# Optimization experiments

Measured on AMD Instinct MI355X. Metric: run time of the kernel, lower is better.

Reference implementation:

```python
import jax, jax.numpy as jnp
import numpy as np

B, S, D = 2, 2048, 1024
H = 16
HD = D // H  # 64
SCALE = HD ** -0.5
EPS = 1e-12  # F.normalize eps


def _rope_sin_cos(length, half, dtype):
    positions = jnp.arange(length, dtype=dtype)
    freqs = jnp.arange(half, dtype=dtype)
    inv_freq = 1.0 / 10000 ** (freqs / max(1, half))
    theta = jnp.einsum('s,f->sf', positions, inv_freq)  # [S, half]
    return jnp.sin(theta)[None, None], jnp.cos(theta)[None, None]  # [1,1,S,half]


def _rotate(x, sin, cos):
    # x: [B,H,S,HD]; interleaved even/odd rotation
    x_even = x[..., 0::2]
    x_odd = x[..., 1::2]
    r_even = x_even * cos - x_odd * sin
    r_odd = x_even * sin + x_odd * cos
    return jnp.stack([r_even, r_odd], axis=-1).reshape(x.shape)


def setup_inputs() -> dict:
    key = jax.random.key(0)
    k1, k2, k3 = jax.random.split(key, 3)
    tokens = jax.random.normal(k1, (B, S, D), dtype=jnp.float32)
    qkv_w = jax.random.normal(k2, (3 * D, D), dtype=jnp.float32) * (D ** -0.5)
    qkv_b = jnp.zeros((3 * D,), dtype=jnp.float32)
    out_w = jax.random.normal(k3, (D, D), dtype=jnp.float32) * (D ** -0.5)
    out_b = jnp.zeros((D,), dtype=jnp.float32)
    return {"tokens": tokens, "qkv_w": qkv_w, "qkv_b": qkv_b,
            "out_w": out_w, "out_b": out_b}


def reference(tokens, qkv_w, qkv_b, out_w, out_b):
    batch, length, _ = tokens.shape
    qkv = tokens @ qkv_w.T + qkv_b                       # [B,S,3D]
    qkv = qkv.reshape(batch, length, 3, H, HD)
    qkv = jnp.transpose(qkv, (0, 3, 1, 2, 4))            # [B,H,S,3,HD]
    q, k, v = qkv[..., 0, :], qkv[..., 1, :], qkv[..., 2, :]
    sin, cos = _rope_sin_cos(length, HD // 2, q.dtype)
    q = _rotate(q, sin, cos)
    k = _rotate(k, sin, cos)
    # QK L2-normalize (F.normalize: x / max(||x||, eps))
    q = q / jnp.maximum(jnp.linalg.norm(q, axis=-1, keepdims=True), EPS)
    k = k / jnp.maximum(jnp.linalg.norm(k, axis=-1, keepdims=True), EPS)
    scores = jnp.einsum('bhqd,bhkd->bhqk', q, k) * SCALE
    attn = jax.nn.softmax(scores, axis=-1)
    out = jnp.einsum('bhqk,bhkd->bhqd', attn, v)          # [B,H,S,HD]
    out = jnp.transpose(out, (0, 2, 1, 3)).reshape(batch, length, D)
    return out @ out_w.T + out_b
```

## Files before the change

kernel.cpp:

```cpp
#include <hip/hip_runtime.h>
#include <hip/hip_bf16.h>
#include <math.h>

#define B_ 2
#define S_ 2048
#define D_ 1024
#define H_ 16
#define HD_ 64
#define BHS (B_*H_*S_)
#define NROWS (B_*S_)

typedef __attribute__((ext_vector_type(8))) short bf16x8;
typedef __attribute__((ext_vector_type(4))) short bf16x4;
typedef __attribute__((ext_vector_type(4))) float f32x4;

#ifdef __HIP_DEVICE_COMPILE__
#if __has_builtin(__builtin_amdgcn_mfma_f32_16x16x16bf16_1k)
#define MFMA16(a, b, c) __builtin_amdgcn_mfma_f32_16x16x16bf16_1k(a, b, c, 0, 0, 0)
#else
#define MFMA16(a, b, c) __builtin_amdgcn_mfma_f32_16x16x16_bf16(a, b, c, 0, 0, 0)
#endif
#define EXP2(x) __builtin_amdgcn_exp2f(x)
#else
#define MFMA16(a, b, c) (c)
#define EXP2(x) exp2f(x)
#endif

#define SCALE_LOG2E 0.18033688011112043f

__device__ __forceinline__ short f2bf(float x) {
  __hip_bfloat16 h = __float2bfloat16(x);
  return *reinterpret_cast<short*>(&h);
}
__device__ __forceinline__ int packbf_hu(float lo, float hi) {
  unsigned lb = __float_as_uint(lo) + 0x8000u;
  unsigned hb = __float_as_uint(hi) + 0x8000u;
  return (int)__builtin_amdgcn_perm(hb, lb, 0x07060302u);
}

__device__ __forceinline__ void gload_lds16(const short* g, short* l) {
  __builtin_amdgcn_global_load_lds(
      (const __attribute__((address_space(1))) void*)g,
      (__attribute__((address_space(3))) void*)l, 16, 0, 0);
}

__global__ __launch_bounds__(256) void prep(
    const float* __restrict__ tokens, const float* __restrict__ qkv_w,
    const float* __restrict__ out_w, short* __restrict__ tok_bf,
    short* __restrict__ qkvw_bf, short* __restrict__ outw_bf,
    float* __restrict__ tab) {
  const int i = blockIdx.x * 256 + threadIdx.x;
  const float* src;
  short* dst;
  int j;
  if (i < 524288) {
    src = tokens; dst = tok_bf; j = i;
  } else if (i < 917504) {
    src = qkv_w; dst = qkvw_bf; j = i - 524288;
  } else if (i < 1048576) {
    src = out_w; dst = outw_bf; j = i - 917504;
  } else if (i < 1056768) {
    const int e = (i - 1048576) * 8;
    const int s = e >> 5;
    const int f0 = e & 31;
#pragma unroll
    for (int k = 0; k < 8; k++) {
      const int f = f0 + k;
      const float theta = (float)s * exp2f(-(float)f * 0.41524101186092034f);
      float sn, cs;
      sincosf(theta, &sn, &cs);
      tab[(s * 32 + f) * 2] = sn;
      tab[(s * 32 + f) * 2 + 1] = cs;
    }
    return;
  } else {
    return;
  }
  const float4 a = *(const float4*)(src + (long)j * 8);
  const float4 b = *(const float4*)(src + (long)j * 8 + 4);
  short tmp[8] = {f2bf(a.x), f2bf(a.y), f2bf(a.z), f2bf(a.w),
                  f2bf(b.x), f2bf(b.y), f2bf(b.z), f2bf(b.w)};
  *(bf16x8*)(dst + (long)j * 8) = *(const bf16x8*)tmp;
}

__global__ __launch_bounds__(256) void qkv_mfma(
    const short* __restrict__ A, const short* __restrict__ W,
    const float* __restrict__ bias, const float* __restrict__ tab,
    short* __restrict__ qb, short* __restrict__ kb, short* __restrict__ vtb) {
  __shared__ short smem[17408];
  short* As = smem;
  short* Bs = smem + 4096;
  const int t = threadIdx.x;
  const int w = t >> 6;
  const int lane = t & 63;
  const int col = lane & 15;
  const int quad = lane >> 4;
  const int wm = w >> 1;
  const int wn = w & 1;
  const int m0 = blockIdx.y * 128;
  const int n0 = blockIdx.x * 128;

  f32x4 acc[4][4] = {};

  for (int k0 = 0; k0 < 1024; k0 += 32) {
    __syncthreads();
#pragma unroll
    for (int i = 0; i < 2; i++) {
      const int c = w * 2 + i;
      const int sl = c * 64 + lane;
      const int row = sl >> 2;
      const int gseg = (sl & 3) ^ (row & 3);
      gload_lds16(&A[(m0 + row) * 1024 + k0 + gseg * 8], As + c * 512);
      gload_lds16(&W[(n0 + row) * 1024 + k0 + gseg * 8], Bs + c * 512);
    }
    __syncthreads();

    bf16x8 af[4], bfr[4];
#pragma unroll
    for (int mt = 0; mt < 4; mt++) {
      const int m = wm * 64 + mt * 16 + col;
      af[mt] = *(const bf16x8*)&As[m * 32 + ((quad ^ (m & 3)) * 8)];
    }
#pragma unroll
    for (int nt = 0; nt < 4; nt++) {
      const int n = wn * 64 + nt * 16 + col;
      bfr[nt] = *(const bf16x8*)&Bs[n * 32 + ((quad ^ (n & 3)) * 8)];
    }
#pragma unroll
    for (int mt = 0; mt < 4; mt++)
#pragma unroll
      for (int nt = 0; nt < 4; nt++)
        acc[mt][nt] = __builtin_amdgcn_mfma_f32_16x16x32_bf16(
            af[mt], bfr[nt], acc[mt][nt], 0, 0, 0);
  }

  const int j_base = n0 + wn * 64;
  const int c = j_base >> 10;
  const int h = (j_base >> 6) & 15;
  float bi[4];
#pragma unroll
  for (int nt = 0; nt < 4; nt++) bi[nt] = bias[j_base + nt * 16 + col];

  __syncthreads();

  if (c < 2) {
    short* dst = (c == 0) ? qb : kb;
    float* Tf = (float*)smem + w * 2176;
#pragma unroll
    for (int half = 0; half < 2; half++) {
#pragma unroll
      for (int mth = 0; mth < 2; mth++) {
        const int mt = half * 2 + mth;
#pragma unroll
        for (int nt = 0; nt < 4; nt++)
#pragma unroll
          for (int r = 0; r < 4; r++)
            Tf[(mth * 16 + quad * 4 + r) * 68 + nt * 16 + col] =
                acc[mt][nt][r] + bi[nt];
      }
#pragma unroll
      for (int p = 0; p < 8; p++) {
        const int rloc = p * 4 + quad;
        const int n = m0 + wm * 64 + half * 32 + rloc;
        const int bidx = n >> 11;
        const int s = n & 2047;
        const float4 xv = *(const float4*)&Tf[rloc * 68 + col * 4];
        const float4 tc = *(const float4*)&tab[s * 64 + col * 4];
        const float e0 = xv.x * tc.y - xv.y * tc.x;
        const float o0 = xv.x * tc.x + xv.y * tc.y;
        const float e1 = xv.z * tc.w - xv.w * tc.z;
        const float o1 = xv.z * tc.z + xv.w * tc.w;
        float ss = e0 * e0 + o0 * o0 + e1 * e1 + o1 * o1;
        ss += __shfl_xor(ss, 1, 64);
        ss += __shfl_xor(ss, 2, 64);
        ss += __shfl_xor(ss, 4, 64);
        ss += __shfl_xor(ss, 8, 64);
        const float scl = 1.0f / fmaxf(sqrtf(ss), 1e-12f);
        int2 pk;
        pk.x = packbf_hu(e0 * scl, o0 * scl);
        pk.y = packbf_hu(e1 * scl, o1 * scl);
        *(int2*)&dst[((long)(bidx * 16 + h) * 2048 + s) * 64 + col * 4] = pk;
      }
    }
  } else {
    const int n64 = m0 + wm * 64;
    const int bidx = n64 >> 11;
    const int st = (n64 & 2047) >> 6;
    short* vbase = vtb + ((long)(bidx * 16 + h) * 32 + st) * 4096;
#pragma unroll
    for (int mt = 0; mt < 4; mt++)
#pragma unroll
      for (int ntq = 0; ntq < 4; ntq++) {
        int2 pk;
        pk.x = packbf_hu(acc[mt][ntq][0] + bi[ntq], acc[mt][ntq][1] + bi[ntq]);
        pk.y = packbf_hu(acc[mt][ntq][2] + bi[ntq], acc[mt][ntq][3] + bi[ntq]);
        *(int2*)&vbase[((mt * 4 + ntq) * 32 + quad * 8 + (col >> 1)) * 8 +
                       (col & 1) * 4] = pk;
      }
  }
}

__global__ __launch_bounds__(512) void attn_mfma(
    const short* __restrict__ qb,
    const short* __restrict__ kb,
    const short* __restrict__ vt,
    short* __restrict__ ob) {
  __shared__ __align__(16) char smem[35328];
  short* Kf = (short*)smem;
  short* Vf = Kf + 8192;
  const int t = threadIdx.x;
  const int w = t >> 6;
  const int grp = w >> 2;
  const int wl = w & 3;
  const int lane = t & 63;
  const int col = lane & 15;
  const int quad = lane >> 4;
  const int bh = blockIdx.x;
  const int q0 = blockIdx.y * 128;
  const long hb = (long)bh * S_ * 64;
  const short* kg = kb + hb;
  const short* vg = vt + (long)bh * 64 * S_;

  bf16x8 qa[2][2];
#pragma unroll
  for (int mt2 = 0; mt2 < 2; mt2++)
#pragma unroll
    for (int h = 0; h < 2; h++)
      qa[mt2][h] = *(const bf16x8*)&qb[hb +
          (long)(q0 + wl * 32 + mt2 * 16 + col) * 64 + h * 32 + quad * 8];

  const int tt = (wl << 6) | lane;
  int kofs[2];
#pragma unroll
  for (int i = 0; i < 2; i++) {
    const int cc = tt + 256 * i;
    kofs[i] = ((cc >> 7) * 16 + (cc & 15)) * 64 + ((cc >> 6) & 1) * 32 +
              ((cc >> 4) & 3) * 8;
  }

  short* KfL = Kf + grp * 4096;
  short* VfL = Vf + grp * 4096;

  f32x4 oacc[2][4] = {};
  f32x4 lacc[2] = {};
  const short oneb = 0x3F80;
  const bf16x4 ones = {oneb, oneb, oneb, oneb};

  const int kend = grp * 1024 + 1024;
  for (int kt = grp * 1024; kt < kend; kt += 64) {
    __syncthreads();
    const short* kgp = kg + (long)kt * 64;
    const short* vgp = vg + (long)(kt >> 6) * 4096;
#pragma unroll
    for (int i = 0; i < 2; i++) {
      gload_lds16(kgp + kofs[i], KfL + i * 2048 + wl * 512);
      gload_lds16(vgp + (tt + 256 * i) * 8, VfL + i * 2048 + wl * 512);
    }
    __syncthreads();

#pragma unroll
    for (int nt = 0; nt < 4; nt++) {
      const bf16x8 ka0 = *(const bf16x8*)&KfL[nt * 1024 + quad * 128 + col * 8];
      const bf16x8 ka1 =
          *(const bf16x8*)&KfL[nt * 1024 + 512 + quad * 128 + col * 8];
      bf16x4 pb[2];
#pragma unroll
      for (int mt2 = 0; mt2 < 2; mt2++) {
        f32x4 z = {0.f, 0.f, 0.f, 0.f};
        z = __builtin_amdgcn_mfma_f32_16x16x32_bf16(ka0, qa[mt2][0], z, 0, 0, 0);
        z = __builtin_amdgcn_mfma_f32_16x16x32_bf16(ka1, qa[mt2][1], z, 0, 0, 0);
        const float e0 = EXP2(z[0] * SCALE_LOG2E);
        const float e1 = EXP2(z[1] * SCALE_LOG2E);
        const float e2 = EXP2(z[2] * SCALE_LOG2E);
        const float e3 = EXP2(z[3] * SCALE_LOG2E);
        int pk[2] = {packbf_hu(e0, e1), packbf_hu(e2, e3)};
        pb[mt2] = *(const bf16x4*)pk;
        lacc[mt2] = MFMA16(ones, pb[mt2], lacc[mt2]);
      }
#pragma unroll
      for (int dt = 0; dt < 4; dt++) {
        const bf16x4 va =
            *(const bf16x4*)&VfL[(nt * 4 + dt) * 256 + quad * 64 + col * 4];
        oacc[0][dt] = MFMA16(va, pb[0], oacc[0][dt]);
        oacc[1][dt] = MFMA16(va, pb[1], oacc[1][dt]);
      }
    }
  }

  __syncthreads();

  float* Ocomb = (float*)smem;
  float* lsumC = (float*)(smem + 34816);
  if (grp == 1) {
#pragma unroll
    for (int mt2 = 0; mt2 < 2; mt2++) {
      const int qloc = wl * 32 + mt2 * 16 + col;
      if (quad == 0) lsumC[qloc] = lacc[mt2][0];
#pragma unroll
      for (int dt = 0; dt < 4; dt++)
        *(f32x4*)&Ocomb[qloc * 68 + dt * 16 + quad * 4] = oacc[mt2][dt];
    }
  }
  __syncthreads();
  if (grp == 0) {
#pragma unroll
    for (int mt2 = 0; mt2 < 2; mt2++) {
      const int qloc = wl * 32 + mt2 * 16 + col;
      const float inv = 1.0f / (lacc[mt2][0] + lsumC[qloc]);
      short* orow = ob + hb + (long)(q0 + qloc) * 64;
#pragma unroll
      for (int dt = 0; dt < 4; dt++) {
        const float4 oc = *(const float4*)&Ocomb[qloc * 68 + dt * 16 + quad * 4];
        int2 pk;
        pk.x = packbf_hu((oacc[mt2][dt][0] + oc.x) * inv,
                         (oacc[mt2][dt][1] + oc.y) * inv);
        pk.y = packbf_hu((oacc[mt2][dt][2] + oc.z) * inv,
                         (oacc[mt2][dt][3] + oc.w) * inv);
        *(int2*)&orow[dt * 16 + quad * 4] = pk;
      }
    }
  }
}

__global__ __launch_bounds__(256) void out_mfma(
    const short* __restrict__ O, const short* __restrict__ W,
    const float* __restrict__ bias, float* __restrict__ out) {
  __shared__ short As[64 * 32];
  __shared__ short Bs[128 * 32];
  const int t = threadIdx.x;
  const int w = t >> 6;
  const int lane = t & 63;
  const int col = lane & 15;
  const int quad = lane >> 4;
  const int wm = w >> 1;
  const int wn = w & 1;
  const int m0 = blockIdx.y * 64;
  const int n0 = blockIdx.x * 128;

  f32x4 acc[2][4] = {};

  for (int k0 = 0; k0 < 1024; k0 += 32) {
    __syncthreads();
    {
      const int row = t >> 2;
      const int gseg = (t & 3) ^ (row & 3);
      const int n = m0 + row;
      const int bidx = n >> 11;
      const int s = n & 2047;
      const int kk = k0 + gseg * 8;
      gload_lds16(&O[((long)(bidx * 16 + (kk >> 6)) * 2048 + s) * 64 + (kk & 63)],
                  As + w * 512);
    }
#pragma unroll
    for (int i = 0; i < 2; i++) {
      const int cs = w * 2 + i;
      const int sl = cs * 64 + lane;
      const int row = sl >> 2;
      const int gseg = (sl & 3) ^ (row & 3);
      gload_lds16(&W[(n0 + row) * 1024 + k0 + gseg * 8], Bs + cs * 512);
    }
    __syncthreads();

    bf16x8 af[2], bfr[4];
#pragma unroll
    for (int mt = 0; mt < 2; mt++) {
      const int m = wm * 32 + mt * 16 + col;
      af[mt] = *(const bf16x8*)&As[m * 32 + ((quad ^ (m & 3)) * 8)];
    }
#pragma unroll
    for (int nt = 0; nt < 4; nt++) {
      const int n = wn * 64 + nt * 16 + col;
      bfr[nt] = *(const bf16x8*)&Bs[n * 32 + ((quad ^ (n & 3)) * 8)];
    }
#pragma unroll
    for (int mt = 0; mt < 2; mt++)
#pragma unroll
      for (int nt = 0; nt < 4; nt++)
        acc[mt][nt] = __builtin_amdgcn_mfma_f32_16x16x32_bf16(
            af[mt], bfr[nt], acc[mt][nt], 0, 0, 0);
  }

  float bi[4];
#pragma unroll
  for (int nt = 0; nt < 4; nt++) bi[nt] = bias[n0 + wn * 64 + nt * 16 + col];
#pragma unroll
  for (int mt = 0; mt < 2; mt++) {
#pragma unroll
    for (int r = 0; r < 4; r++) {
      const int n = m0 + wm * 32 + mt * 16 + quad * 4 + r;
#pragma unroll
      for (int nt = 0; nt < 4; nt++)
        out[(long)n * 1024 + n0 + wn * 64 + nt * 16 + col] =
            acc[mt][nt][r] + bi[nt];
    }
  }
}

extern "C" void kernel_launch(void* const* d_in, const int* in_sizes, int n_in,
                              void* d_out, int out_size, void* d_ws,
                              size_t ws_size, hipStream_t stream) {
  const float* tokens = (const float*)d_in[0];
  const float* qkv_w = (const float*)d_in[1];
  const float* qkv_b = (const float*)d_in[2];
  const float* out_w = (const float*)d_in[3];
  const float* out_b = (const float*)d_in[4];
  float* out = (float*)d_out;

  const size_t per = (size_t)BHS * HD_;
  float* tab = (float*)d_ws;
  short* tok_bf = (short*)(tab + 2048 * 64);
  short* qkvw_bf = tok_bf + per;
  short* outw_bf = qkvw_bf + 3 * per / 4;
  short* q_bf = outw_bf + per / 4;
  short* k_bf = q_bf + per;
  short* vt_bf = k_bf + per;
  short* O_bf = vt_bf + per;

  hipLaunchKernelGGL(prep, dim3(4128), dim3(256), 0, stream, tokens, qkv_w,
                     out_w, tok_bf, qkvw_bf, outw_bf, tab);
  hipLaunchKernelGGL(qkv_mfma, dim3(24, 32), dim3(256), 0, stream, tok_bf,
                     qkvw_bf, qkv_b, tab, q_bf, k_bf, vt_bf);
  hipLaunchKernelGGL(attn_mfma, dim3(B_ * H_, S_ / 128), dim3(512), 0, stream,
                     q_bf, k_bf, vt_bf, O_bf);
  hipLaunchKernelGGL(out_mfma, dim3(8, 64), dim3(256), 0, stream, O_bf,
                     outw_bf, out_b, out);
}
```

Baseline: 208.3 us.

## Shrink GEMM tiles and remap block IDs for XCD-local weight reuse

The QKV projection tile shrinks from 128x128 to 64x128 and the output projection tile from 64x128 to 64x64, which raises the block count to 1536 and 1024 so all CUs stay busy. Both launches become 1-D grids whose block index is decoded so that blocks landing on the same XCD share a narrow range of weight columns, aiming for better L2 reuse. The epilogues (RoPE, normalise, V-transpose store) are adjusted to the smaller tiles. Smaller tiles give less reuse per block and more redundant loads of A.

```diff
diff --git a/kernel.cpp b/kernel.cpp
--- a/kernel.cpp
+++ b/kernel.cpp
@@ -87,9 +87,9 @@
     const short* __restrict__ A, const short* __restrict__ W,
     const float* __restrict__ bias, const float* __restrict__ tab,
     short* __restrict__ qb, short* __restrict__ kb, short* __restrict__ vtb) {
-  __shared__ short smem[17408];
+  __shared__ short smem[8704];
   short* As = smem;
-  short* Bs = smem + 4096;
+  short* Bs = smem + 2048;
   const int t = threadIdx.x;
   const int w = t >> 6;
   const int lane = t & 63;
@@ -97,28 +97,36 @@
   const int quad = lane >> 4;
   const int wm = w >> 1;
   const int wn = w & 1;
-  const int m0 = blockIdx.y * 128;
-  const int n0 = blockIdx.x * 128;
-
-  f32x4 acc[4][4] = {};
+  const int bid = blockIdx.x;
+  const int xcd = bid & 7;
+  const int seq = bid >> 3;
+  const int m0 = (seq / 3) * 64;
+  const int n0 = (xcd * 3 + seq % 3) * 128;
+
+  f32x4 acc[2][4] = {};
 
   for (int k0 = 0; k0 < 1024; k0 += 32) {
     __syncthreads();
+    {
+      const int c = w * 64 + lane;
+      const int row = c >> 2;
+      const int gseg = (c & 3) ^ (row & 3);
+      gload_lds16(&A[(m0 + row) * 1024 + k0 + gseg * 8], As + w * 512);
+    }
 #pragma unroll
     for (int i = 0; i < 2; i++) {
-      const int c = w * 2 + i;
-      const int sl = c * 64 + lane;
-      const int row = sl >> 2;
-      const int gseg = (sl & 3) ^ (row & 3);
-      gload_lds16(&A[(m0 + row) * 1024 + k0 + gseg * 8], As + c * 512);
-      gload_lds16(&W[(n0 + row) * 1024 + k0 + gseg * 8], Bs + c * 512);
-    }
-    __syncthreads();
-
-    bf16x8 af[4], bfr[4];
-#pragma unroll
-    for (int mt = 0; mt < 4; mt++) {
-      const int m = wm * 64 + mt * 16 + col;
+      const int c0 = i * 256 + w * 64;
+      const int c = c0 + lane;
+      const int row = c >> 2;
+      const int gseg = (c & 3) ^ (row & 3);
+      gload_lds16(&W[(n0 + row) * 1024 + k0 + gseg * 8], Bs + c0 * 8);
+    }
+    __syncthreads();
+
+    bf16x8 af[2], bfr[4];
+#pragma unroll
+    for (int mt = 0; mt < 2; mt++) {
+      const int m = wm * 32 + mt * 16 + col;
       af[mt] = *(const bf16x8*)&As[m * 32 + ((quad ^ (m & 3)) * 8)];
     }
 #pragma unroll
@@ -127,7 +135,7 @@
       bfr[nt] = *(const bf16x8*)&Bs[n * 32 + ((quad ^ (n & 3)) * 8)];
     }
 #pragma unroll
-    for (int mt = 0; mt < 4; mt++)
+    for (int mt = 0; mt < 2; mt++)
 #pragma unroll
       for (int nt = 0; nt < 4; nt++)
         acc[mt][nt] = __builtin_amdgcn_mfma_f32_16x16x32_bf16(
@@ -145,23 +153,18 @@
 
   if (c < 2) {
     short* dst = (c == 0) ? qb : kb;
-    float* Tf = (float*)smem + w * 2176;
-#pragma unroll
-    for (int half = 0; half < 2; half++) {
-#pragma unroll
-      for (int mth = 0; mth < 2; mth++) {
-        const int mt = half * 2 + mth;
-#pragma unroll
-        for (int nt = 0; nt < 4; nt++)
-#pragma unroll
-          for (int r = 0; r < 4; r++)
-            Tf[(mth * 16 + quad * 4 + r) * 68 + nt * 16 + col] =
-                acc[mt][nt][r] + bi[nt];
-      }
-#pragma unroll
-      for (int p = 0; p < 8; p++) {
+    float* Tf = (float*)smem + w * 1088;
+#pragma unroll
+    for (int mt = 0; mt < 2; mt++) {
+#pragma unroll
+      for (int nt = 0; nt < 4; nt++)
+#pragma unroll
+        for (int r = 0; r < 4; r++)
+          Tf[(quad * 4 + r) * 68 + nt * 16 + col] = acc[mt][nt][r] + bi[nt];
+#pragma unroll
+      for (int p = 0; p < 4; p++) {
         const int rloc = p * 4 + quad;
-        const int n = m0 + wm * 64 + half * 32 + rloc;
+        const int n = m0 + wm * 32 + mt * 16 + rloc;
         const int bidx = n >> 11;
         const int s = n & 2047;
         const float4 xv = *(const float4*)&Tf[rloc * 68 + col * 4];
@@ -183,19 +186,18 @@
       }
     }
   } else {
-    const int n64 = m0 + wm * 64;
-    const int bidx = n64 >> 11;
-    const int st = (n64 & 2047) >> 6;
+    const int bidx = m0 >> 11;
+    const int st = (m0 & 2047) >> 6;
     short* vbase = vtb + ((long)(bidx * 16 + h) * 32 + st) * 4096;
 #pragma unroll
-    for (int mt = 0; mt < 4; mt++)
+    for (int mt = 0; mt < 2; mt++)
 #pragma unroll
       for (int ntq = 0; ntq < 4; ntq++) {
         int2 pk;
         pk.x = packbf_hu(acc[mt][ntq][0] + bi[ntq], acc[mt][ntq][1] + bi[ntq]);
         pk.y = packbf_hu(acc[mt][ntq][2] + bi[ntq], acc[mt][ntq][3] + bi[ntq]);
-        *(int2*)&vbase[((mt * 4 + ntq) * 32 + quad * 8 + (col >> 1)) * 8 +
-                       (col & 1) * 4] = pk;
+        *(int2*)&vbase[(((wm * 2 + mt) * 4 + ntq) * 32 + quad * 8 +
+                        (col >> 1)) * 8 + (col & 1) * 4] = pk;
       }
   }
 }
@@ -325,8 +327,8 @@
 __global__ __launch_bounds__(256) void out_mfma(
     const short* __restrict__ O, const short* __restrict__ W,
     const float* __restrict__ bias, float* __restrict__ out) {
-  __shared__ short As[64 * 32];
-  __shared__ short Bs[128 * 32];
+  __shared__ short As[2048];
+  __shared__ short Bs[2048];
   const int t = threadIdx.x;
   const int w = t >> 6;
   const int lane = t & 63;
@@ -334,16 +336,20 @@
   const int quad = lane >> 4;
   const int wm = w >> 1;
   const int wn = w & 1;
-  const int m0 = blockIdx.y * 64;
-  const int n0 = blockIdx.x * 128;
-
-  f32x4 acc[2][4] = {};
+  const int bid = blockIdx.x;
+  const int xcd = bid & 7;
+  const int seq = bid >> 3;
+  const int m0 = (seq >> 1) * 64;
+  const int n0 = (xcd * 2 + (seq & 1)) * 64;
+
+  f32x4 acc[2][2] = {};
 
   for (int k0 = 0; k0 < 1024; k0 += 32) {
     __syncthreads();
     {
-      const int row = t >> 2;
-      const int gseg = (t & 3) ^ (row & 3);
+      const int c = w * 64 + lane;
+      const int row = c >> 2;
+      const int gseg = (c & 3) ^ (row & 3);
       const int n = m0 + row;
       const int bidx = n >> 11;
       const int s = n & 2047;
@@ -351,46 +357,44 @@
       gload_lds16(&O[((long)(bidx * 16 + (kk >> 6)) * 2048 + s) * 64 + (kk & 63)],
                   As + w * 512);
     }
-#pragma unroll
-    for (int i = 0; i < 2; i++) {
-      const int cs = w * 2 + i;
-      const int sl = cs * 64 + lane;
-      const int row = sl >> 2;
-      const int gseg = (sl & 3) ^ (row & 3);
-      gload_lds16(&W[(n0 + row) * 1024 + k0 + gseg * 8], Bs + cs * 512);
-    }
-    __syncthreads();
-
-    bf16x8 af[2], bfr[4];
+    {
+      const int c = w * 64 + lane;
+      const int row = c >> 2;
+      const int gseg = (c & 3) ^ (row & 3);
+      gload_lds16(&W[(n0 + row) * 1024 + k0 + gseg * 8], Bs + w * 512);
+    }
+    __syncthreads();
+
+    bf16x8 af[2], bfr[2];
 #pragma unroll
     for (int mt = 0; mt < 2; mt++) {
       const int m = wm * 32 + mt * 16 + col;
       af[mt] = *(const bf16x8*)&As[m * 32 + ((quad ^ (m & 3)) * 8)];
     }
 #pragma unroll
-    for (int nt = 0; nt < 4; nt++) {
-      const int n = wn * 64 + nt * 16 + col;
+    for (int nt = 0; nt < 2; nt++) {
+      const int n = wn * 32 + nt * 16 + col;
       bfr[nt] = *(const bf16x8*)&Bs[n * 32 + ((quad ^ (n & 3)) * 8)];
     }
 #pragma unroll
     for (int mt = 0; mt < 2; mt++)
 #pragma unroll
-      for (int nt = 0; nt < 4; nt++)
+      for (int nt = 0; nt < 2; nt++)
         acc[mt][nt] = __builtin_amdgcn_mfma_f32_16x16x32_bf16(
             af[mt], bfr[nt], acc[mt][nt], 0, 0, 0);
   }
 
-  float bi[4];
-#pragma unroll
-  for (int nt = 0; nt < 4; nt++) bi[nt] = bias[n0 + wn * 64 + nt * 16 + col];
+  float bi[2];
+#pragma unroll
+  for (int nt = 0; nt < 2; nt++) bi[nt] = bias[n0 + wn * 32 + nt * 16 + col];
 #pragma unroll
   for (int mt = 0; mt < 2; mt++) {
 #pragma unroll
     for (int r = 0; r < 4; r++) {
       const int n = m0 + wm * 32 + mt * 16 + quad * 4 + r;
 #pragma unroll
-      for (int nt = 0; nt < 4; nt++)
-        out[(long)n * 1024 + n0 + wn * 64 + nt * 16 + col] =
+      for (int nt = 0; nt < 2; nt++)
+        out[(long)n * 1024 + n0 + wn * 32 + nt * 16 + col] =
             acc[mt][nt][r] + bi[nt];
     }
   }
@@ -418,10 +422,10 @@
 
   hipLaunchKernelGGL(prep, dim3(4128), dim3(256), 0, stream, tokens, qkv_w,
                      out_w, tok_bf, qkvw_bf, outw_bf, tab);
-  hipLaunchKernelGGL(qkv_mfma, dim3(24, 32), dim3(256), 0, stream, tok_bf,
+  hipLaunchKernelGGL(qkv_mfma, dim3(1536), dim3(256), 0, stream, tok_bf,
                      qkvw_bf, qkv_b, tab, q_bf, k_bf, vt_bf);
   hipLaunchKernelGGL(attn_mfma, dim3(B_ * H_, S_ / 128), dim3(512), 0, stream,
                      q_bf, k_bf, vt_bf, O_bf);
-  hipLaunchKernelGGL(out_mfma, dim3(8, 64), dim3(256), 0, stream, O_bf,
+  hipLaunchKernelGGL(out_mfma, dim3(1024), dim3(256), 0, stream, O_bf,
                      outw_bf, out_b, out);
 }
```

Measured after the change: 201.9 us. -3.0%, faster.
